# Kernel optimization log

Hardware: AMD Instinct MI355X
Metric: run time of the kernel (lower is better)

The kernel has to match this reference:

```python
import jax, jax.numpy as jnp
import numpy as np


def setup_inputs() -> dict:
    key = jax.random.key(0)
    k1, k2, k3 = jax.random.split(key, 3)
    B, T1, T2, D, MP = 16, 256, 256, 256, 32
    reps_lt = jax.random.normal(k1, (B, T1, D), dtype=jnp.float32)
    reps_rt = jax.random.normal(k2, (B, T2, D), dtype=jnp.float32)
    # keras 'uniform' initializer ~ U(-0.05, 0.05); stored as [mp, d]
    kernel = jax.random.uniform(k3, (MP, D), dtype=jnp.float32, minval=-0.05, maxval=0.05)
    return {"reps_lt": reps_lt, "reps_rt": reps_rt, "kernel": kernel}


def reference(reps_lt, reps_rt, kernel):
    # reps_lt: [b, t1, d], reps_rt: [b, t2, d], kernel: [mp, d]
    # Original: broadcast lt*kernel -> [b,t1,1,mp,d], rt -> [b,1,t2,1,d],
    # cosine_norm=False => tanh(sum over d), then max over t1.
    lt_m = reps_lt[:, :, None, :] * kernel[None, None, :, :]      # [b, t1, mp, d]
    scores = jnp.einsum('bimd,bjd->bijm', lt_m, reps_rt)           # [b, t1, t2, mp]
    match = jnp.tanh(scores)
    return jnp.max(match, axis=1)                                  # [b, t2, mp]
```

## Files before the change

kernel.cpp:

```cpp
#include <hip/hip_runtime.h>
#include <hip/hip_bf16.h>
#include <math.h>

#define Bn   16
#define T1n  256
#define T2n  256
#define Dn   256
#define MPn  32

typedef __attribute__((ext_vector_type(8))) short short8;
typedef __attribute__((ext_vector_type(4))) float f32x4;

typedef const __attribute__((address_space(1))) void* gp_t;
typedef __attribute__((address_space(3))) void* lp_t;

__device__ __forceinline__ void gl_lds16(const void* g, void* l) {
  __builtin_amdgcn_global_load_lds((gp_t)g, (lp_t)l, 16, 0, 0);
}

__device__ inline short f2b(float f) {
  __hip_bfloat16 h = __float2bfloat16(f);
  return __builtin_bit_cast(short, h);
}
__device__ inline float b2f(short s) {
  unsigned int u = ((unsigned int)(unsigned short)s) << 16;
  return __builtin_bit_cast(float, u);
}

__device__ inline int swz_chunk(int row, int d8) {
  return row * 32 + (d8 ^ (row & 7));
}

__global__ __launch_bounds__(256, 8)
void cvt_bf16_kernel(const float* __restrict__ lt, const float* __restrict__ rt,
                     short* __restrict__ olt, short* __restrict__ ort) {
  int blk = blockIdx.x;
  const float* src;
  short* dst;
  int t;
  if (blk < 512) { src = lt; dst = olt; t = blk * 256 + threadIdx.x; }
  else           { src = rt; dst = ort; t = (blk - 512) * 256 + threadIdx.x; }
  const f32x4* s = reinterpret_cast<const f32x4*>(src + (size_t)t * 8);
  f32x4 f0 = s[0], f1 = s[1];
  short8 v;
  v[0] = f2b(f0.x); v[1] = f2b(f0.y); v[2] = f2b(f0.z); v[3] = f2b(f0.w);
  v[4] = f2b(f1.x); v[5] = f2b(f1.y); v[6] = f2b(f1.z); v[7] = f2b(f1.w);
  *reinterpret_cast<short8*>(dst + (size_t)t * 8) = v;
}

__global__ __launch_bounds__(512, 2)
void mp_match_kernel(const short* __restrict__ ltb,
                     const short* __restrict__ rtb,
                     const float* __restrict__ kern,
                     float* __restrict__ out) {
  __shared__ short lds_rt[64 * 256];
  __shared__ short lds_lt[2][64 * 256];

  const int bid  = blockIdx.x;
  const int xcd  = bid & 7;
  const int q    = bid >> 3;
  const int widx = q & 15;
  const int b    = ((q >> 4) << 3) | xcd;
  const int jblk = widx & 3;
  const int mg   = widx >> 2;
  const int j0   = jblk * 64;

  const int tid  = threadIdx.x;
  const int lane = tid & 63;
  const int w    = tid >> 6;
  const int m    = mg * 8 + w;
  const int bl   = lane & 15;
  const int hl   = lane >> 4;

  int soff[4];
  #pragma unroll
  for (int it = 0; it < 4; ++it) {
    int cidx = it * 512 + tid;
    int row = cidx >> 5, slot = cidx & 31;
    int c = slot ^ (row & 7);
    soff[it] = row * 256 + c * 8;
  }
  const int cb0 = (tid & ~63) * 8;

  const short* rbase = rtb + ((size_t)b * T2n + j0) * Dn;
  #pragma unroll
  for (int it = 0; it < 4; ++it)
    gl_lds16(rbase + soff[it], &lds_rt[it * 512 * 8 + cb0]);
  asm volatile("s_waitcnt vmcnt(0)" ::: "memory");
  __syncthreads();

  const short* lbase = ltb + (size_t)b * T1n * Dn;
  #pragma unroll
  for (int it = 0; it < 4; ++it)
    gl_lds16(lbase + soff[it], &lds_lt[0][it * 512 * 8 + cb0]);

  short8 bsc[4][8];
  {
    const float* kbase = kern + (size_t)m * Dn;
    #pragma unroll
    for (int kk = 0; kk < 8; ++kk) {
      int d8 = kk * 4 + hl;
      const f32x4* kp = reinterpret_cast<const f32x4*>(kbase + d8 * 8);
      f32x4 k0 = kp[0], k1 = kp[1];
      #pragma unroll
      for (int sub = 0; sub < 4; ++sub) {
        int brow = sub * 16 + bl;
        short8 r = *reinterpret_cast<const short8*>(&lds_rt[swz_chunk(brow, d8) * 8]);
        short8 v;
        v[0] = f2b(b2f(r[0]) * k0.x); v[1] = f2b(b2f(r[1]) * k0.y);
        v[2] = f2b(b2f(r[2]) * k0.z); v[3] = f2b(b2f(r[3]) * k0.w);
        v[4] = f2b(b2f(r[4]) * k1.x); v[5] = f2b(b2f(r[5]) * k1.y);
        v[6] = f2b(b2f(r[6]) * k1.z); v[7] = f2b(b2f(r[7]) * k1.w);
        bsc[sub][kk] = v;
      }
    }
  }

  float jmax0 = -1e30f, jmax1 = -1e30f, jmax2 = -1e30f, jmax3 = -1e30f;

  asm volatile("s_waitcnt vmcnt(0)" ::: "memory");
  __syncthreads();

  for (int ic = 0; ic < 4; ++ic) {
    const int cur = ic & 1;
    if (ic < 3) {
      #pragma unroll
      for (int it = 0; it < 4; ++it)
        gl_lds16(lbase + (ic + 1) * 64 * 256 + soff[it],
                 &lds_lt[cur ^ 1][it * 512 * 8 + cb0]);
    }
    const short* lcur = lds_lt[cur];
    #pragma unroll
    for (int it2 = 0; it2 < 4; ++it2) {
      f32x4 acc0 = {0.f,0.f,0.f,0.f}, acc1 = {0.f,0.f,0.f,0.f};
      f32x4 acc2 = {0.f,0.f,0.f,0.f}, acc3 = {0.f,0.f,0.f,0.f};
      int arow = it2 * 16 + bl;
      #pragma unroll
      for (int kk = 0; kk < 8; ++kk) {
        int d8 = kk * 4 + hl;
        short8 a = *reinterpret_cast<const short8*>(&lcur[swz_chunk(arow, d8) * 8]);
        acc0 = __builtin_amdgcn_mfma_f32_16x16x32_bf16(a, bsc[0][kk], acc0, 0, 0, 0);
        acc1 = __builtin_amdgcn_mfma_f32_16x16x32_bf16(a, bsc[1][kk], acc1, 0, 0, 0);
        acc2 = __builtin_amdgcn_mfma_f32_16x16x32_bf16(a, bsc[2][kk], acc2, 0, 0, 0);
        acc3 = __builtin_amdgcn_mfma_f32_16x16x32_bf16(a, bsc[3][kk], acc3, 0, 0, 0);
      }
      jmax0 = fmaxf(jmax0, fmaxf(fmaxf(acc0.x, acc0.y), fmaxf(acc0.z, acc0.w)));
      jmax1 = fmaxf(jmax1, fmaxf(fmaxf(acc1.x, acc1.y), fmaxf(acc1.z, acc1.w)));
      jmax2 = fmaxf(jmax2, fmaxf(fmaxf(acc2.x, acc2.y), fmaxf(acc2.z, acc2.w)));
      jmax3 = fmaxf(jmax3, fmaxf(fmaxf(acc3.x, acc3.y), fmaxf(acc3.z, acc3.w)));
    }
    if (ic < 3) {
      asm volatile("s_waitcnt vmcnt(0)" ::: "memory");
      __syncthreads();
    }
  }

  jmax0 = fmaxf(jmax0, __shfl_xor(jmax0, 16));
  jmax0 = fmaxf(jmax0, __shfl_xor(jmax0, 32));
  jmax1 = fmaxf(jmax1, __shfl_xor(jmax1, 16));
  jmax1 = fmaxf(jmax1, __shfl_xor(jmax1, 32));
  jmax2 = fmaxf(jmax2, __shfl_xor(jmax2, 16));
  jmax2 = fmaxf(jmax2, __shfl_xor(jmax2, 32));
  jmax3 = fmaxf(jmax3, __shfl_xor(jmax3, 16));
  jmax3 = fmaxf(jmax3, __shfl_xor(jmax3, 32));
  float v = (hl == 0) ? jmax0 : (hl == 1) ? jmax1 : (hl == 2) ? jmax2 : jmax3;
  int j = j0 + hl * 16 + bl;
  out[((size_t)b * T2n + j) * MPn + m] = tanhf(v);
}

extern "C" void kernel_launch(void* const* d_in, const int* in_sizes, int n_in,
                              void* d_out, int out_size, void* d_ws, size_t ws_size,
                              hipStream_t stream) {
  const float* lt   = (const float*)d_in[0];
  const float* rt   = (const float*)d_in[1];
  const float* kern = (const float*)d_in[2];
  float* out = (float*)d_out;

  short* ltb = (short*)d_ws;
  short* rtb = ltb + (size_t)Bn * T1n * Dn;

  cvt_bf16_kernel<<<1024, 256, 0, stream>>>(lt, rt, ltb, rtb);
  mp_match_kernel<<<256, 512, 0, stream>>>(ltb, rtb, kern, out);
}
```

Baseline: 26.70 us.

## Shrink match tiles to 32 j-rows and 4 mp per block, launch 1024 blocks

```diff
diff --git a/kernel.cpp b/kernel.cpp
--- a/kernel.cpp
+++ b/kernel.cpp
@@ -26,6 +26,9 @@
   unsigned int u = ((unsigned int)(unsigned short)s) << 16;
   return __builtin_bit_cast(float, u);
 }
+__device__ inline float max4(f32x4 a) {
+  return fmaxf(fmaxf(a.x, a.y), fmaxf(a.z, a.w));
+}
 
 __device__ inline int swz_chunk(int row, int d8) {
   return row * 32 + (d8 ^ (row & 7));
@@ -48,53 +51,52 @@
   *reinterpret_cast<short8*>(dst + (size_t)t * 8) = v;
 }
 
-__global__ __launch_bounds__(512, 2)
+__global__ __launch_bounds__(256, 3)
 void mp_match_kernel(const short* __restrict__ ltb,
                      const short* __restrict__ rtb,
                      const float* __restrict__ kern,
                      float* __restrict__ out) {
-  __shared__ short lds_rt[64 * 256];
-  __shared__ short lds_lt[2][64 * 256];
+  __shared__ short lds_rt[32 * 256];
+  __shared__ short lds_lt[2][32 * 256];
 
-  const int bid  = blockIdx.x;
-  const int xcd  = bid & 7;
-  const int q    = bid >> 3;
-  const int widx = q & 15;
-  const int b    = ((q >> 4) << 3) | xcd;
-  const int jblk = widx & 3;
-  const int mg   = widx >> 2;
-  const int j0   = jblk * 64;
+  const int bid = blockIdx.x;
+  const int xcd = bid & 7;
+  const int idx = bid >> 3;
+  const int b   = ((idx >> 6) << 3) | xcd;
+  const int rem = idx & 63;
+  const int jblk = rem & 7;
+  const int mg   = rem >> 3;
+  const int j0   = jblk * 32;
 
   const int tid  = threadIdx.x;
   const int lane = tid & 63;
   const int w    = tid >> 6;
-  const int m    = mg * 8 + w;
+  const int m    = mg * 4 + w;
   const int bl   = lane & 15;
   const int hl   = lane >> 4;
 
   int soff[4];
   #pragma unroll
   for (int it = 0; it < 4; ++it) {
-    int cidx = it * 512 + tid;
+    int cidx = it * 256 + tid;
     int row = cidx >> 5, slot = cidx & 31;
-    int c = slot ^ (row & 7);
-    soff[it] = row * 256 + c * 8;
+    soff[it] = row * 256 + (slot ^ (row & 7)) * 8;
   }
-  const int cb0 = (tid & ~63) * 8;
+  const int wub = (tid & ~63) * 8;
 
   const short* rbase = rtb + ((size_t)b * T2n + j0) * Dn;
   #pragma unroll
   for (int it = 0; it < 4; ++it)
-    gl_lds16(rbase + soff[it], &lds_rt[it * 512 * 8 + cb0]);
+    gl_lds16(rbase + soff[it], &lds_rt[it * 256 * 8 + wub]);
   asm volatile("s_waitcnt vmcnt(0)" ::: "memory");
   __syncthreads();
 
   const short* lbase = ltb + (size_t)b * T1n * Dn;
   #pragma unroll
   for (int it = 0; it < 4; ++it)
-    gl_lds16(lbase + soff[it], &lds_lt[0][it * 512 * 8 + cb0]);
+    gl_lds16(lbase + soff[it], &lds_lt[0][it * 256 * 8 + wub]);
 
-  short8 bsc[4][8];
+  short8 bsc[2][8];
   {
     const float* kbase = kern + (size_t)m * Dn;
     #pragma unroll
@@ -103,7 +105,7 @@
       const f32x4* kp = reinterpret_cast<const f32x4*>(kbase + d8 * 8);
       f32x4 k0 = kp[0], k1 = kp[1];
       #pragma unroll
-      for (int sub = 0; sub < 4; ++sub) {
+      for (int sub = 0; sub < 2; ++sub) {
         int brow = sub * 16 + bl;
         short8 r = *reinterpret_cast<const short8*>(&lds_rt[swz_chunk(brow, d8) * 8]);
         short8 v;
@@ -116,40 +118,35 @@
     }
   }
 
-  float jmax0 = -1e30f, jmax1 = -1e30f, jmax2 = -1e30f, jmax3 = -1e30f;
+  float jmax0 = -1e30f, jmax1 = -1e30f;
 
   asm volatile("s_waitcnt vmcnt(0)" ::: "memory");
   __syncthreads();
 
-  for (int ic = 0; ic < 4; ++ic) {
+  for (int ic = 0; ic < 8; ++ic) {
     const int cur = ic & 1;
-    if (ic < 3) {
+    if (ic < 7) {
       #pragma unroll
       for (int it = 0; it < 4; ++it)
-        gl_lds16(lbase + (ic + 1) * 64 * 256 + soff[it],
-                 &lds_lt[cur ^ 1][it * 512 * 8 + cb0]);
+        gl_lds16(lbase + (ic + 1) * 32 * 256 + soff[it],
+                 &lds_lt[cur ^ 1][it * 256 * 8 + wub]);
     }
     const short* lcur = lds_lt[cur];
+    f32x4 a00 = {0.f,0.f,0.f,0.f}, a01 = {0.f,0.f,0.f,0.f};
+    f32x4 a10 = {0.f,0.f,0.f,0.f}, a11 = {0.f,0.f,0.f,0.f};
     #pragma unroll
-    for (int it2 = 0; it2 < 4; ++it2) {
-      f32x4 acc0 = {0.f,0.f,0.f,0.f}, acc1 = {0.f,0.f,0.f,0.f};
-      f32x4 acc2 = {0.f,0.f,0.f,0.f}, acc3 = {0.f,0.f,0.f,0.f};
-      int arow = it2 * 16 + bl;
-      #pragma unroll
-      for (int kk = 0; kk < 8; ++kk) {
-        int d8 = kk * 4 + hl;
-        short8 a = *reinterpret_cast<const short8*>(&lcur[swz_chunk(arow, d8) * 8]);
-        acc0 = __builtin_amdgcn_mfma_f32_16x16x32_bf16(a, bsc[0][kk], acc0, 0, 0, 0);
-        acc1 = __builtin_amdgcn_mfma_f32_16x16x32_bf16(a, bsc[1][kk], acc1, 0, 0, 0);
-        acc2 = __builtin_amdgcn_mfma_f32_16x16x32_bf16(a, bsc[2][kk], acc2, 0, 0, 0);
-        acc3 = __builtin_amdgcn_mfma_f32_16x16x32_bf16(a, bsc[3][kk], acc3, 0, 0, 0);
-      }
-      jmax0 = fmaxf(jmax0, fmaxf(fmaxf(acc0.x, acc0.y), fmaxf(acc0.z, acc0.w)));
-      jmax1 = fmaxf(jmax1, fmaxf(fmaxf(acc1.x, acc1.y), fmaxf(acc1.z, acc1.w)));
-      jmax2 = fmaxf(jmax2, fmaxf(fmaxf(acc2.x, acc2.y), fmaxf(acc2.z, acc2.w)));
-      jmax3 = fmaxf(jmax3, fmaxf(fmaxf(acc3.x, acc3.y), fmaxf(acc3.z, acc3.w)));
+    for (int kk = 0; kk < 8; ++kk) {
+      int d8 = kk * 4 + hl;
+      short8 A0 = *reinterpret_cast<const short8*>(&lcur[swz_chunk(bl, d8) * 8]);
+      short8 A1 = *reinterpret_cast<const short8*>(&lcur[swz_chunk(16 + bl, d8) * 8]);
+      a00 = __builtin_amdgcn_mfma_f32_16x16x32_bf16(A0, bsc[0][kk], a00, 0, 0, 0);
+      a01 = __builtin_amdgcn_mfma_f32_16x16x32_bf16(A0, bsc[1][kk], a01, 0, 0, 0);
+      a10 = __builtin_amdgcn_mfma_f32_16x16x32_bf16(A1, bsc[0][kk], a10, 0, 0, 0);
+      a11 = __builtin_amdgcn_mfma_f32_16x16x32_bf16(A1, bsc[1][kk], a11, 0, 0, 0);
     }
-    if (ic < 3) {
+    jmax0 = fmaxf(jmax0, fmaxf(max4(a00), max4(a10)));
+    jmax1 = fmaxf(jmax1, fmaxf(max4(a01), max4(a11)));
+    if (ic < 7) {
       asm volatile("s_waitcnt vmcnt(0)" ::: "memory");
       __syncthreads();
     }
@@ -159,13 +156,11 @@
   jmax0 = fmaxf(jmax0, __shfl_xor(jmax0, 32));
   jmax1 = fmaxf(jmax1, __shfl_xor(jmax1, 16));
   jmax1 = fmaxf(jmax1, __shfl_xor(jmax1, 32));
-  jmax2 = fmaxf(jmax2, __shfl_xor(jmax2, 16));
-  jmax2 = fmaxf(jmax2, __shfl_xor(jmax2, 32));
-  jmax3 = fmaxf(jmax3, __shfl_xor(jmax3, 16));
-  jmax3 = fmaxf(jmax3, __shfl_xor(jmax3, 32));
-  float v = (hl == 0) ? jmax0 : (hl == 1) ? jmax1 : (hl == 2) ? jmax2 : jmax3;
-  int j = j0 + hl * 16 + bl;
-  out[((size_t)b * T2n + j) * MPn + m] = tanhf(v);
+  if (hl < 2) {
+    float v = hl ? jmax1 : jmax0;
+    int j = j0 + hl * 16 + bl;
+    out[((size_t)b * T2n + j) * MPn + m] = tanhf(v);
+  }
 }
 
 extern "C" void kernel_launch(void* const* d_in, const int* in_sizes, int n_in,
@@ -180,5 +175,5 @@
   short* rtb = ltb + (size_t)Bn * T1n * Dn;
 
   cvt_bf16_kernel<<<1024, 256, 0, stream>>>(lt, rt, ltb, rtb);
-  mp_match_kernel<<<256, 512, 0, stream>>>(ltb, rtb, kern, out);
+  mp_match_kernel<<<1024, 256, 0, stream>>>(ltb, rtb, kern, out);
 }
```

New measurement: 28.68 us. 1.07x slower.
